# Kernel optimization log

Measured on AMD Instinct MI355X. Metric: run time of the kernel, lower is better.

Reference implementation:

```python
import jax, jax.numpy as jnp
import numpy as np

B, P, L1, D = 64, 16, 16, 1024  # images, people/img, object slots/img (slot0=no-object), feat dim
SP = 32   # flattened spatial (Conv_spatial output channels)
PROJ = 512
ACT = 29


def setup_inputs() -> dict:
    key = jax.random.key(0)
    ks = jax.random.split(key, 16)
    rn = lambda k, s, sc=1.0: jax.random.normal(k, s, dtype=jnp.float32) * sc
    w = 0.02  # weight init scale
    return {
        "people": rn(ks[0], (B, P, D)),
        "objects": rn(ks[1], (B, L1, D)),
        "context": rn(ks[2], (B, D)),
        "spatial": rn(ks[3], (B, P * L1, SP)),
        "Wvis_w": rn(ks[4], (3 * D, PROJ), w), "Wvis_b": jnp.zeros((PROJ,), jnp.float32),
        "Wspat_w": rn(ks[5], (SP, PROJ), w), "Wspat_b": jnp.zeros((PROJ,), jnp.float32),
        "Wip_w": rn(ks[6], (PROJ, 1), w), "Wip_b": jnp.zeros((1,), jnp.float32),
        "Wref_w": rn(ks[7], (PROJ, ACT), w), "Wref_b": jnp.zeros((ACT,), jnp.float32),
        "Watt_w": rn(ks[8], (PROJ, ACT), w), "Watt_b": jnp.zeros((ACT,), jnp.float32),
        "Woh_w": rn(ks[9], (D, D), w), "Woh_b": jnp.zeros((D,), jnp.float32),
        "Who_w": rn(ks[10], (D, D), w), "Who_b": jnp.zeros((D,), jnp.float32),
        "Wg_w": rn(ks[11], (2 * D, ACT), w), "Wg_b": jnp.zeros((ACT,), jnp.float32),
    }


def reference(people, objects, context, spatial,
              Wvis_w, Wvis_b, Wspat_w, Wspat_b, Wip_w, Wip_b,
              Wref_w, Wref_b, Watt_w, Watt_b,
              Woh_w, Woh_b, Who_w, Who_b, Wg_w, Wg_b):
    Bn, Pn, Dn = people.shape
    L = objects.shape[1]
    C = Bn * Pn * L

    # --- ROI.pairing: all (person, object-slot) pairs + image context -> [C, 3D]
    pe = jnp.broadcast_to(people[:, :, None, :], (Bn, Pn, L, Dn))
    ob = jnp.broadcast_to(objects[:, None, :, :], (Bn, Pn, L, Dn))
    cx = jnp.broadcast_to(context[:, None, None, :], (Bn, Pn, L, Dn))
    pairs = jnp.concatenate([pe, ob, cx], axis=-1).reshape(C, 3 * Dn)

    # --- attention / visual projection heads
    a_ho = jax.nn.relu(spatial.reshape(C, -1) @ Wspat_w + Wspat_b)   # W_Spat
    f_vis = jax.nn.relu(pairs @ Wvis_w + Wvis_b)                     # W_vis
    f_ref = f_vis * a_ho
    i_ho = f_ref @ Wip_w + Wip_b                                     # [C,1]
    interaction_prob = jax.nn.sigmoid(i_ho)
    p_ref = f_ref @ Wref_w + Wref_b                                  # [C,29]
    p_att = a_ho @ Watt_w + Watt_b                                   # [C,29]

    # --- graph message passing: adjacency = interaction probs, skipping slot 0 (no-object)
    adj = interaction_prob.reshape(Bn, Pn, L)[:, :, 1:]              # [B,P,O]
    oh = jax.nn.relu(objects[:, 1:] @ Woh_w + Woh_b)                 # W_oh on objects
    ho = jax.nn.relu(people @ Who_w + Who_b)                         # W_ho on people
    people_r = people + jnp.einsum('bpo,bod->bpd', adj, oh)
    objects_r = objects[:, 1:] + jnp.einsum('bpo,bpd->bod', adj, ho)
    objects_full = jnp.concatenate([objects[:, :1], objects_r], axis=1)  # re-attach no-object slot

    # --- refined all-pairs concat -> W_graph
    pe_r = jnp.broadcast_to(people_r[:, :, None, :], (Bn, Pn, L, Dn))
    ob_r = jnp.broadcast_to(objects_full[:, None, :, :], (Bn, Pn, L, Dn))
    pairs_g = jnp.concatenate([pe_r, ob_r], axis=-1).reshape(C, 2 * Dn)
    p_graph = pairs_g @ Wg_w + Wg_b                                  # [C,29]

    return (i_ho, p_ref, p_att, p_graph)
```

## Files before the change

### kernel.cpp

```cpp
#include <hip/hip_runtime.h>


typedef unsigned short u16;
typedef short s16x8 __attribute__((ext_vector_type(8)));
typedef float f32x4 __attribute__((ext_vector_type(4)));

__device__ __forceinline__ u16 f2b(float f) {
    union { float f; unsigned int i; } v; v.f = f;
    unsigned int r = (v.i + 0x7fffu + ((v.i >> 16) & 1u)) >> 16;
    return (u16)r;
}
__device__ __forceinline__ float b2f(u16 u) {
    union { float f; unsigned int i; } v; v.i = ((unsigned int)u) << 16; return v.f;
}
__device__ __forceinline__ unsigned int pack2(float x, float y) {
    return (unsigned int)f2b(x) | ((unsigned int)f2b(y) << 16);
}

#define OFF_WSPATT 0u
#define OFF_WREFT  32768u
#define OFF_WATTT  65536u
#define OFF_WGT    98304u
#define OFF_PP     229376u
#define OFF_PO     1277952u
#define OFF_PC     2326528u
#define OFF_ADJ    2392064u
#define OFF_HP     2457600u
#define OFF_HOF    2588672u
#define OFF_YH     2719744u
#define OFF_ZO     2850816u
#define ZERO_OFF   2457600u
#define ZERO_LEN   516096u
#define OFF_WVIST2 2973696u
#define OFF_WHOT2  6119424u
#define OFF_WOHT2  8216576u
#define OFF_PEOB   10313728u
#define OFF_OBJB   12410880u
#define OFF_CTXB   14508032u
#define OFF_SPATB  14639104u
#define OFF_AHOB   15687680u

__global__ __launch_bounds__(256) void prep_all(
    const float* __restrict__ people, const float* __restrict__ objects,
    const float* __restrict__ context, const float* __restrict__ spatial,
    const float* __restrict__ Wvis, const float* __restrict__ Who,
    const float* __restrict__ Woh, const float* __restrict__ Wspat,
    const float* __restrict__ Wref, const float* __restrict__ Watt,
    const float* __restrict__ Wg,
    u16* __restrict__ peoB, u16* __restrict__ objB, u16* __restrict__ ctxB,
    u16* __restrict__ spatB, u16* __restrict__ WvisT, u16* __restrict__ WhoT,
    u16* __restrict__ WohT, u16* __restrict__ WspatT, u16* __restrict__ WrefT,
    u16* __restrict__ WattT, u16* __restrict__ WgT, float* __restrict__ zeroWS)
{
    __shared__ float S[64][65];
    int bid = blockIdx.x, t = threadIdx.x;
    if (bid < 896) {
        const float* src; u16* dst; int N, K, kt, nt;
        int tb = bid;
        if (tb < 256)      { src = Who;  dst = WhoT;  K = 1024; N = 1024; kt = tb >> 4; nt = tb & 15; }
        else if (tb < 512) { tb -= 256; src = Woh;  dst = WohT;  K = 1024; N = 1024; kt = tb >> 4; nt = tb & 15; }
        else               { tb -= 512; src = Wvis; dst = WvisT; K = 3072; N = 512;  kt = tb >> 3; nt = tb & 7; }
        int k0 = kt * 64, n0 = nt * 64;
        int r = t >> 4, c4 = (t & 15) * 4;
#pragma unroll
        for (int i = 0; i < 4; i++) {
            float4 v = *(const float4*)&src[(size_t)(k0 + r + 16 * i) * N + n0 + c4];
            S[r + 16 * i][c4 + 0] = v.x;
            S[r + 16 * i][c4 + 1] = v.y;
            S[r + 16 * i][c4 + 2] = v.z;
            S[r + 16 * i][c4 + 3] = v.w;
        }
        __syncthreads();
#pragma unroll
        for (int i = 0; i < 4; i++) {
            int nn = r + 16 * i;
            unsigned int lo = pack2(S[c4 + 0][nn], S[c4 + 1][nn]);
            unsigned int hi = pack2(S[c4 + 2][nn], S[c4 + 3][nn]);
            *(uint2*)&dst[(size_t)(n0 + nn) * K + k0 + c4] = make_uint2(lo, hi);
        }
        return;
    }
    int g = (bid - 896) * 256 + t;
    const int gsz = 512 * 256;
    for (int i = g; i < 262144; i += gsz) {
        float4 v = ((const float4*)people)[i];
        ((uint2*)peoB)[i] = make_uint2(pack2(v.x, v.y), pack2(v.z, v.w));
    }
    for (int i = g; i < 262144; i += gsz) {
        float4 v = ((const float4*)objects)[i];
        ((uint2*)objB)[i] = make_uint2(pack2(v.x, v.y), pack2(v.z, v.w));
    }
    for (int i = g; i < 16384; i += gsz) {
        float4 v = ((const float4*)context)[i];
        ((uint2*)ctxB)[i] = make_uint2(pack2(v.x, v.y), pack2(v.z, v.w));
    }
    for (int i = g; i < 131072; i += gsz) {
        float4 v = ((const float4*)spatial)[i];
        ((uint2*)spatB)[i] = make_uint2(pack2(v.x, v.y), pack2(v.z, v.w));
    }
    for (int i = g; i < 32256; i += gsz) {
        f32x4 z = {0.f, 0.f, 0.f, 0.f};
        ((f32x4*)zeroWS)[i] = z;
    }
    for (int i = g; i < 512 * 32; i += gsz) {
        int n = i >> 5, k = i & 31;
        WspatT[i] = f2b(Wspat[k * 512 + n]);
    }
    for (int i = g; i < 32 * 512; i += gsz) {
        int n = i >> 9, k = i & 511;
        WrefT[i] = (n < 29) ? f2b(Wref[k * 29 + n]) : (u16)0;
        WattT[i] = (n < 29) ? f2b(Watt[k * 29 + n]) : (u16)0;
    }
    for (int i = g; i < 32 * 2048; i += gsz) {
        int n = i >> 11, k = i & 2047;
        WgT[i] = (n < 29) ? f2b(Wg[k * 29 + n]) : (u16)0;
    }
}

__global__ __launch_bounds__(256) void fused_gemms(
    const u16* __restrict__ peoB, const u16* __restrict__ objB,
    const u16* __restrict__ ctxB, const u16* __restrict__ WvisT,
    const u16* __restrict__ WhoT, const float* __restrict__ Who_b,
    const u16* __restrict__ WohT, const float* __restrict__ Woh_b,
    const u16* __restrict__ WgT,
    const u16* __restrict__ spatB, const u16* __restrict__ WspatT,
    const float* __restrict__ bspat,
    const u16* __restrict__ WattT, const float* __restrict__ batt,
    u16* __restrict__ Pp, u16* __restrict__ Po, u16* __restrict__ Pc,
    float* __restrict__ Yh, float* __restrict__ Zo,
    float* __restrict__ Hp, float* __restrict__ HoF,
    u16* __restrict__ ahoB, float* __restrict__ outAtt)
{
    __shared__ __align__(16) unsigned char LB[36864];
    u16 (*As)[64][72] = (u16(*)[64][72])LB;
    u16 (*Bs)[64][72] = (u16(*)[64][72])(LB + 18432);

    int b0 = blockIdx.x, bid;
    if (b0 < 264)      bid = (b0 & 7) * 33 + (b0 >> 3);
    else if (b0 < 760) { int l = b0 - 264; bid = 264 + (l & 7) * 62 + (l >> 3); }
    else if (b0 < 888) { int l = b0 - 760; bid = 760 + (l & 7) * 16 + (l >> 3); }
    else               { int l = b0 - 888; bid = 888 + (l & 7) * 64 + (l >> 3); }
    int t = threadIdx.x;
    int lane = t & 63, w = t >> 6;
    int l16 = lane & 15, q = lane >> 4;
    int wy = w >> 1, wx = w & 1;

    if (bid < 760) {
        const u16 *Ap, *Bp;
        int Bstride, bm, bn, koff = 0, zrm = 0;
        u16* outB = nullptr;
        const float* bb = nullptr; const u16* Wg2 = nullptr; float* U = nullptr;
        if (bid < 264) {
            int bx = bid & 7, ty = bid >> 3;
            if (ty < 16)      { Ap = peoB; outB = Pp; koff = 0;    bm = ty * 64; }
            else if (ty < 32) { Ap = objB; outB = Po; koff = 1024; bm = (ty - 16) * 64; }
            else              { Ap = ctxB; outB = Pc; koff = 2048; bm = 0; }
            bn = bx * 64;
            Bp = WvisT; Bstride = 3072;
        } else {
            int r3 = bid - 264;
            int zz, rt, nbt;
            if (r3 < 256) { zz = 0; rt = r3 >> 4; nbt = r3 & 15; }
            else          { zz = 1; r3 -= 256; rt = r3 >> 4; nbt = r3 & 15; }
            zrm = zz;
            Ap = zz ? objB : peoB;
            Bp = zz ? WohT : WhoT; Bstride = 1024;
            bb = zz ? Woh_b : Who_b;
            Wg2 = zz ? WgT : WgT + 1024;
            U = zz ? Zo : Yh;
            bm = rt * 64; bn = nbt * 64;
        }

        int tr = t >> 3, tc = (t & 7) * 8;
        int a0r = bm + tr, a1r = bm + 32 + tr;
        if (zrm) { a0r = (a0r / 15) * 16 + (a0r % 15) + 1;
                   a1r = (a1r / 15) * 16 + (a1r % 15) + 1; }
        const u16* gA0 = Ap + (size_t)a0r * 1024 + tc;
        const u16* gA1 = Ap + (size_t)a1r * 1024 + tc;
        const u16* gB0 = Bp + (size_t)(bn + tr) * Bstride + koff + tc;
        const u16* gB1 = Bp + (size_t)(bn + 32 + tr) * Bstride + koff + tc;

        s16x8 rA0 = *(const s16x8*)gA0, rA1 = *(const s16x8*)gA1;
        s16x8 rB0 = *(const s16x8*)gB0, rB1 = *(const s16x8*)gB1;
        gA0 += 64; gA1 += 64; gB0 += 64; gB1 += 64;
        *(s16x8*)&As[0][tr][tc]      = rA0;
        *(s16x8*)&As[0][32 + tr][tc] = rA1;
        *(s16x8*)&Bs[0][tr][tc]      = rB0;
        *(s16x8*)&Bs[0][32 + tr][tc] = rB1;
        rA0 = *(const s16x8*)gA0; rA1 = *(const s16x8*)gA1;
        rB0 = *(const s16x8*)gB0; rB1 = *(const s16x8*)gB1;
        gA0 += 64; gA1 += 64; gB0 += 64; gB1 += 64;
        __syncthreads();

        f32x4 acc00 = {0,0,0,0}, acc01 = {0,0,0,0}, acc10 = {0,0,0,0}, acc11 = {0,0,0,0};
        int cur = 0;
        for (int kt = 0; kt < 16; kt++) {
#pragma unroll
            for (int kk = 0; kk < 2; kk++) {
                s16x8 a0 = *(const s16x8*)&As[cur][wy * 32 + l16][kk * 32 + q * 8];
                s16x8 a1 = *(const s16x8*)&As[cur][wy * 32 + 16 + l16][kk * 32 + q * 8];
                s16x8 b0 = *(const s16x8*)&Bs[cur][wx * 32 + l16][kk * 32 + q * 8];
                s16x8 b1 = *(const s16x8*)&Bs[cur][wx * 32 + 16 + l16][kk * 32 + q * 8];
                acc00 = __builtin_amdgcn_mfma_f32_16x16x32_bf16(a0, b0, acc00, 0, 0, 0);
                acc01 = __builtin_amdgcn_mfma_f32_16x16x32_bf16(a0, b1, acc01, 0, 0, 0);
                acc10 = __builtin_amdgcn_mfma_f32_16x16x32_bf16(a1, b0, acc10, 0, 0, 0);
                acc11 = __builtin_amdgcn_mfma_f32_16x16x32_bf16(a1, b1, acc11, 0, 0, 0);
            }
            if (kt < 15) {
                __syncthreads();
                *(s16x8*)&As[cur ^ 1][tr][tc]      = rA0;
                *(s16x8*)&As[cur ^ 1][32 + tr][tc] = rA1;
                *(s16x8*)&Bs[cur ^ 1][tr][tc]      = rB0;
                *(s16x8*)&Bs[cur ^ 1][32 + tr][tc] = rB1;
                if (kt < 14) {
                    rA0 = *(const s16x8*)gA0; rA1 = *(const s16x8*)gA1;
                    rB0 = *(const s16x8*)gB0; rB1 = *(const s16x8*)gB1;
                    gA0 += 64; gA1 += 64; gB0 += 64; gB1 += 64;
                }
                __syncthreads();
                cur ^= 1;
            }
        }

        f32x4 accs[2][2] = {{acc00, acc01}, {acc10, acc11}};
        if (bid < 264) {
#pragma unroll
            for (int ii = 0; ii < 2; ii++)
#pragma unroll
                for (int jj = 0; jj < 2; jj++) {
                    int col = bn + wx * 32 + jj * 16 + l16;
#pragma unroll
                    for (int r = 0; r < 4; r++) {
                        int row = bm + wy * 32 + ii * 16 + q * 4 + r;
                        outB[(size_t)row * 512 + col] = f2b(accs[ii][jj][r]);
                    }
                }
        } else {
            u16 (*T)[72] = As[0];
#pragma unroll
            for (int ii = 0; ii < 2; ii++)
#pragma unroll
                for (int jj = 0; jj < 2; jj++) {
                    int col = wx * 32 + jj * 16 + l16;
                    float bv = bb[bn + col];
#pragma unroll
                    for (int rr = 0; rr < 4; rr++) {
                        float v = accs[ii][jj][rr] + bv;
                        T[wy * 32 + ii * 16 + q * 4 + rr][col] = f2b(fmaxf(v, 0.f));
                    }
                }
            __syncthreads();

            f32x4 s20 = {0,0,0,0}, s21 = {0,0,0,0};
#pragma unroll
            for (int kk = 0; kk < 64; kk += 32) {
                s16x8 a2 = *(const s16x8*)(&T[w * 16 + l16][kk + q * 8]);
                s16x8 b20 = *(const s16x8*)(Wg2 + (size_t)l16 * 2048 + bn + kk + q * 8);
                s16x8 b21 = *(const s16x8*)(Wg2 + (size_t)(16 + l16) * 2048 + bn + kk + q * 8);
                s20 = __builtin_amdgcn_mfma_f32_16x16x32_bf16(a2, b20, s20, 0, 0, 0);
                s21 = __builtin_amdgcn_mfma_f32_16x16x32_bf16(a2, b21, s21, 0, 0, 0);
            }
#pragma unroll
            for (int rr = 0; rr < 4; rr++) {
                int row = bm + w * 16 + q * 4 + rr;
                atomicAdd(&U[(size_t)row * 32 + l16], s20[rr]);
                atomicAdd(&U[(size_t)row * 32 + 16 + l16], s21[rr]);
            }
        }
    } else if (bid < 888) {
        int r3 = bid - 760;
        int bx = r3 & 7, by = (r3 >> 3) & 7, z = r3 >> 6;
        const u16* A  = z ? objB : peoB;
        const u16* BT = z ? WgT + 1024 : WgT;
        float* outF   = z ? HoF : Hp;
        int bm = bx * 128 + w * 32;
        int kb = by * 128;
        const u16* ap0 = A + (size_t)(bm + l16) * 1024 + kb + q * 8;
        const u16* ap1 = A + (size_t)(bm + 16 + l16) * 1024 + kb + q * 8;
        const u16* bp0 = BT + (size_t)l16 * 2048 + kb + q * 8;
        const u16* bp1 = BT + (size_t)(16 + l16) * 2048 + kb + q * 8;
        f32x4 acc00 = {0,0,0,0}, acc01 = {0,0,0,0}, acc10 = {0,0,0,0}, acc11 = {0,0,0,0};
        s16x8 bA0[4], bA1[4], bB0[4], bB1[4];
#pragma unroll
        for (int s = 0; s < 4; s++) {
            bA0[s] = *(const s16x8*)(ap0 + s * 32);
            bA1[s] = *(const s16x8*)(ap1 + s * 32);
            bB0[s] = *(const s16x8*)(bp0 + s * 32);
            bB1[s] = *(const s16x8*)(bp1 + s * 32);
        }
#pragma unroll
        for (int s = 0; s < 4; s++) {
            acc00 = __builtin_amdgcn_mfma_f32_16x16x32_bf16(bA0[s], bB0[s], acc00, 0, 0, 0);
            acc01 = __builtin_amdgcn_mfma_f32_16x16x32_bf16(bA0[s], bB1[s], acc01, 0, 0, 0);
            acc10 = __builtin_amdgcn_mfma_f32_16x16x32_bf16(bA1[s], bB0[s], acc10, 0, 0, 0);
            acc11 = __builtin_amdgcn_mfma_f32_16x16x32_bf16(bA1[s], bB1[s], acc11, 0, 0, 0);
        }
        f32x4 accs[2][2] = {{acc00, acc01}, {acc10, acc11}};
#pragma unroll
        for (int ii = 0; ii < 2; ii++)
#pragma unroll
            for (int jj = 0; jj < 2; jj++)
#pragma unroll
                for (int r = 0; r < 4; r++)
                    atomicAdd(&outF[(size_t)(bm + ii * 16 + q * 4 + r) * 32 + jj * 16 + l16],
                              accs[ii][jj][r]);
    } else {
        u16 (*tile)[512] = (u16(*)[512])LB;
        int c0 = (bid - 888) * 32;

        {
            s16x8 a0 = *(const s16x8*)(spatB + (size_t)(c0 + l16) * 32 + q * 8);
            s16x8 a1 = *(const s16x8*)(spatB + (size_t)(c0 + 16 + l16) * 32 + q * 8);
            const u16* wb = WspatT + (size_t)(w * 128 + l16) * 32 + q * 8;
            s16x8 cb = *(const s16x8*)wb;
            s16x8 nb_ = *(const s16x8*)(wb + 16 * 32);
            wb += 32 * 32;
#pragma unroll
            for (int nt = 0; nt < 8; nt++) {
                s16x8 tb;
                if (nt < 6) { tb = *(const s16x8*)wb; wb += 16 * 32; }
                int n = w * 128 + nt * 16;
                f32x4 acc0 = {0,0,0,0}, acc1 = {0,0,0,0};
                acc0 = __builtin_amdgcn_mfma_f32_16x16x32_bf16(a0, cb, acc0, 0, 0, 0);
                acc1 = __builtin_amdgcn_mfma_f32_16x16x32_bf16(a1, cb, acc1, 0, 0, 0);
                cb = nb_; nb_ = tb;
                float bias = bspat[n + l16];
#pragma unroll
                for (int r = 0; r < 4; r++) {
                    tile[q * 4 + r][n + l16]      = f2b(fmaxf(acc0[r] + bias, 0.f));
                    tile[16 + q * 4 + r][n + l16] = f2b(fmaxf(acc1[r] + bias, 0.f));
                }
            }
        }
        __syncthreads();

        {
            int rt = w >> 1, ct = w & 1;
            const u16* bp = WattT + (size_t)(ct * 16 + l16) * 512 + q * 8;
            const u16* ar = &tile[rt * 16 + l16][q * 8];
            f32x4 acc0 = {0,0,0,0}, acc1 = {0,0,0,0}, acc2 = {0,0,0,0}, acc3 = {0,0,0,0};
#pragma unroll
            for (int s = 0; s < 16; s += 4) {
                s16x8 a0 = *(const s16x8*)(ar + (s + 0) * 32);
                s16x8 a1 = *(const s16x8*)(ar + (s + 1) * 32);
                s16x8 a2 = *(const s16x8*)(ar + (s + 2) * 32);
                s16x8 a3 = *(const s16x8*)(ar + (s + 3) * 32);
                s16x8 b0 = *(const s16x8*)(bp + (s + 0) * 32);
                s16x8 b1 = *(const s16x8*)(bp + (s + 1) * 32);
                s16x8 b2 = *(const s16x8*)(bp + (s + 2) * 32);
                s16x8 b3 = *(const s16x8*)(bp + (s + 3) * 32);
                acc0 = __builtin_amdgcn_mfma_f32_16x16x32_bf16(a0, b0, acc0, 0, 0, 0);
                acc1 = __builtin_amdgcn_mfma_f32_16x16x32_bf16(a1, b1, acc1, 0, 0, 0);
                acc2 = __builtin_amdgcn_mfma_f32_16x16x32_bf16(a2, b2, acc2, 0, 0, 0);
                acc3 = __builtin_amdgcn_mfma_f32_16x16x32_bf16(a3, b3, acc3, 0, 0, 0);
            }
            f32x4 acc = (acc0 + acc1) + (acc2 + acc3);
            int col = ct * 16 + l16;
            if (col < 29) {
                float bias = batt[col];
#pragma unroll
                for (int r = 0; r < 4; r++) {
                    int row = c0 + rt * 16 + q * 4 + r;
                    outAtt[(size_t)row * 29 + col] = acc[r] + bias;
                }
            }
        }

        {
            const uint4* ts = (const uint4*)tile;
            uint4* gd = (uint4*)(ahoB + (size_t)c0 * 512);
            for (int i = t; i < 2048; i += 256) gd[i] = ts[i];
        }
    }
}

__global__ __launch_bounds__(256) void mega(
    const u16* __restrict__ ahoB,
    const u16* __restrict__ Pp, const u16* __restrict__ Po,
    const u16* __restrict__ Pc, const float* __restrict__ bvis,
    const u16* __restrict__ WrefT, const float* __restrict__ bref,
    const float* __restrict__ wip, const float* __restrict__ bip,
    float* __restrict__ outI, float* __restrict__ outRef,
    float* __restrict__ adjw)
{
    __shared__ u16 tile[32][512];
    __shared__ float part[32][8];
    __shared__ float wipS[512];
    int t = threadIdx.x;
    int b0 = blockIdx.x;
    int bid = (b0 & 7) * 64 + (b0 >> 3);
    int c0 = bid * 32;
    int lane = t & 63, w = t >> 6;
    int l16 = lane & 15, q = lane >> 4;

    {
        float2 u = *(const float2*)(wip + t * 2);
        wipS[t * 2]     = u.x;
        wipS[t * 2 + 1] = u.y;
    }
    __syncthreads();

    {
        int row = t >> 3, g = t & 7;
        int c = c0 + row;
        int rp = c >> 4, bimg = c >> 8;
        int ro = bimg * 16 + (c & 15);
        const u16* ppr = Pp + (size_t)rp * 512;
        const u16* por = Po + (size_t)ro * 512;
        const u16* pcr = Pc + (size_t)bimg * 512;
        const u16* ahr = ahoB + (size_t)c * 512;
        float ps = 0.f;
#pragma unroll 4
        for (int j = 0; j < 64; j += 2) {
            int col = g * 64 + j;
            unsigned int upp = *(const unsigned int*)(ppr + col);
            unsigned int upo = *(const unsigned int*)(por + col);
            unsigned int upc = *(const unsigned int*)(pcr + col);
            float2 bv = *(const float2*)(bvis + col);
            unsigned int uah = *(const unsigned int*)(ahr + col);
            float fv0 = fmaxf(b2f((u16)(upp & 0xffff)) + b2f((u16)(upo & 0xffff))
                            + b2f((u16)(upc & 0xffff)) + bv.x, 0.f);
            float fv1 = fmaxf(b2f((u16)(upp >> 16)) + b2f((u16)(upo >> 16))
                            + b2f((u16)(upc >> 16)) + bv.y, 0.f);
            float fr0 = fv0 * b2f((u16)(uah & 0xffff));
            float fr1 = fv1 * b2f((u16)(uah >> 16));
            *(unsigned int*)(&tile[row][col]) = pack2(fr0, fr1);
            ps += fr0 * wipS[col] + fr1 * wipS[col + 1];
        }
        part[row][g] = ps;
    }
    __syncthreads();

    if (t < 32) {
        float s = part[t][0] + part[t][1] + part[t][2] + part[t][3]
                + part[t][4] + part[t][5] + part[t][6] + part[t][7] + bip[0];
        outI[c0 + t] = s;
        adjw[c0 + t] = 1.f / (1.f + expf(-s));
    }

    {
        int rt = w >> 1, ct = w & 1;
        const u16* bp = WrefT + (size_t)(ct * 16 + l16) * 512 + q * 8;
        const u16* ar = &tile[rt * 16 + l16][q * 8];
        f32x4 acc0 = {0,0,0,0}, acc1 = {0,0,0,0}, acc2 = {0,0,0,0}, acc3 = {0,0,0,0};
#pragma unroll
        for (int s = 0; s < 16; s += 4) {
            s16x8 a0 = *(const s16x8*)(ar + (s + 0) * 32);
            s16x8 a1 = *(const s16x8*)(ar + (s + 1) * 32);
            s16x8 a2 = *(const s16x8*)(ar + (s + 2) * 32);
            s16x8 a3 = *(const s16x8*)(ar + (s + 3) * 32);
            s16x8 b0 = *(const s16x8*)(bp + (s + 0) * 32);
            s16x8 b1 = *(const s16x8*)(bp + (s + 1) * 32);
            s16x8 b2 = *(const s16x8*)(bp + (s + 2) * 32);
            s16x8 b3 = *(const s16x8*)(bp + (s + 3) * 32);
            acc0 = __builtin_amdgcn_mfma_f32_16x16x32_bf16(a0, b0, acc0, 0, 0, 0);
            acc1 = __builtin_amdgcn_mfma_f32_16x16x32_bf16(a1, b1, acc1, 0, 0, 0);
            acc2 = __builtin_amdgcn_mfma_f32_16x16x32_bf16(a2, b2, acc2, 0, 0, 0);
            acc3 = __builtin_amdgcn_mfma_f32_16x16x32_bf16(a3, b3, acc3, 0, 0, 0);
        }
        f32x4 acc = (acc0 + acc1) + (acc2 + acc3);
        int col = ct * 16 + l16;
        if (col < 29) {
            float bias = bref[col];
#pragma unroll
            for (int r = 0; r < 4; r++) {
                int row = c0 + rt * 16 + q * 4 + r;
                outRef[(size_t)row * 29 + col] = acc[r] + bias;
            }
        }
    }
}

__global__ __launch_bounds__(256) void pgraph2(
    const float* __restrict__ adjw, const float* __restrict__ Hp,
    const float* __restrict__ HoF, const float* __restrict__ Yh,
    const float* __restrict__ Zo, const float* __restrict__ bg,
    float* __restrict__ outG)
{
    int b = blockIdx.x, t = threadIdx.x;
    __shared__ float adjS[16][16];
    __shared__ float YhS[16][32];
    __shared__ float ZoS[15][32];
    __shared__ float PA[16][32];
    __shared__ float OA[16][32];
    adjS[t >> 4][t & 15] = adjw[b * 256 + t];
    for (int i = t; i < 512; i += 256)
        YhS[i >> 5][i & 31] = Yh[(size_t)(b * 16 + (i >> 5)) * 32 + (i & 31)];
    for (int i = t; i < 480; i += 256)
        ZoS[i >> 5][i & 31] = Zo[(size_t)(b * 15 + (i >> 5)) * 32 + (i & 31)];
    __syncthreads();
    for (int i = t; i < 512; i += 256) {
        int p = i >> 5, j = i & 31;
        float s = 0.f;
#pragma unroll
        for (int o = 0; o < 15; o++) s += adjS[p][o + 1] * ZoS[o][j];
        PA[p][j] = s;
        float s2 = 0.f;
#pragma unroll
        for (int pp = 0; pp < 16; pp++) s2 += adjS[pp][p] * YhS[pp][j];
        OA[p][j] = s2;
    }
    __syncthreads();
    int p = t >> 4, l = t & 15;
    const float* hp = Hp + (size_t)(b * 16 + p) * 32;
    const float* ho = HoF + (size_t)(b * 16 + l) * 32;
    size_t c = (size_t)b * 256 + t;
    for (int j = 0; j < 29; j++) {
        float v = hp[j] + ho[j] + bg[j] + PA[p][j];
        if (l >= 1) v += OA[l][j];
        outG[c * 29 + j] = v;
    }
}

extern "C" void kernel_launch(void* const* d_in, const int* in_sizes, int n_in,
                              void* d_out, int out_size, void* d_ws, size_t ws_size,
                              hipStream_t stream)
{
    const float* people  = (const float*)d_in[0];
    const float* objects = (const float*)d_in[1];
    const float* context = (const float*)d_in[2];
    const float* spatial = (const float*)d_in[3];
    const float* Wvis_w  = (const float*)d_in[4];
    const float* Wvis_b  = (const float*)d_in[5];
    const float* Wspat_w = (const float*)d_in[6];
    const float* Wspat_b = (const float*)d_in[7];
    const float* Wip_w   = (const float*)d_in[8];
    const float* Wip_b   = (const float*)d_in[9];
    const float* Wref_w  = (const float*)d_in[10];
    const float* Wref_b  = (const float*)d_in[11];
    const float* Watt_w  = (const float*)d_in[12];
    const float* Watt_b  = (const float*)d_in[13];
    const float* Woh_w   = (const float*)d_in[14];
    const float* Woh_b   = (const float*)d_in[15];
    const float* Who_w   = (const float*)d_in[16];
    const float* Who_b   = (const float*)d_in[17];
    const float* Wg_w    = (const float*)d_in[18];
    const float* Wg_b    = (const float*)d_in[19];

    char* ws = (char*)d_ws;
    u16* WspatT = (u16*)(ws + OFF_WSPATT);
    u16* WrefT  = (u16*)(ws + OFF_WREFT);
    u16* WattT  = (u16*)(ws + OFF_WATTT);
    u16* WgT    = (u16*)(ws + OFF_WGT);
    u16* Ppb    = (u16*)(ws + OFF_PP);
    u16* Pob    = (u16*)(ws + OFF_PO);
    u16* Pcb    = (u16*)(ws + OFF_PC);
    float* adjw = (float*)(ws + OFF_ADJ);
    float* Hp   = (float*)(ws + OFF_HP);
    float* HoF  = (float*)(ws + OFF_HOF);
    float* Yh   = (float*)(ws + OFF_YH);
    float* Zo   = (float*)(ws + OFF_ZO);
    u16* WvisT2 = (u16*)(ws + OFF_WVIST2);
    u16* WhoT2  = (u16*)(ws + OFF_WHOT2);
    u16* WohT2  = (u16*)(ws + OFF_WOHT2);
    u16* peoB   = (u16*)(ws + OFF_PEOB);
    u16* objB   = (u16*)(ws + OFF_OBJB);
    u16* ctxB   = (u16*)(ws + OFF_CTXB);
    u16* spatB  = (u16*)(ws + OFF_SPATB);
    u16* ahoB   = (u16*)(ws + OFF_AHOB);
    float* zeroWS = (float*)(ws + ZERO_OFF);

    float* outI   = (float*)d_out;
    float* outRef = outI + 16384;
    float* outAtt = outI + 491520;
    float* outG   = outI + 966656;

    prep_all<<<1408, 256, 0, stream>>>(people, objects, context, spatial,
        Wvis_w, Who_w, Woh_w, Wspat_w, Wref_w, Watt_w, Wg_w,
        peoB, objB, ctxB, spatB, WvisT2, WhoT2, WohT2,
        WspatT, WrefT, WattT, WgT, zeroWS);

    fused_gemms<<<1400, 256, 0, stream>>>(peoB, objB, ctxB, WvisT2,
        WhoT2, Who_b, WohT2, Woh_b, WgT,
        spatB, WspatT, Wspat_b, WattT, Watt_b,
        Ppb, Pob, Pcb, Yh, Zo, Hp, HoF,
        ahoB, outAtt);

    mega<<<512, 256, 0, stream>>>(ahoB,
                                  Ppb, Pob, Pcb, Wvis_b,
                                  WrefT, Wref_b,
                                  Wip_w, Wip_b,
                                  outI, outRef, adjw);

    pgraph2<<<64, 256, 0, stream>>>(adjw, Hp, HoF, Yh, Zo, Wg_b, outG);
}
```

Before: 156.6 us.

## Stage GEMM tiles via direct global-to-LDS loads with XOR-swizzled layout

Replaces the register-staged double-buffered GEMM loads in the main fused_gemms path with global_load_lds direct copies into LDS. The padded 72-column layout becomes an unpadded 64-column layout with an XOR swizzle, which is meant to avoid bank conflicts and save LDS. This cuts register pressure and VGPR round-trips and removes one barrier per k-step. It relies on the async load having completed by the single __syncthreads, which is a correctness risk if no explicit vmcnt wait is emitted.

```diff
diff --git a/kernel.cpp b/kernel.cpp
--- a/kernel.cpp
+++ b/kernel.cpp
@@ -15,6 +15,12 @@
 }
 __device__ __forceinline__ unsigned int pack2(float x, float y) {
     return (unsigned int)f2b(x) | ((unsigned int)f2b(y) << 16);
+}
+
+typedef __attribute__((address_space(1))) const unsigned int GU1;
+typedef __attribute__((address_space(3))) unsigned int LU3;
+__device__ __forceinline__ void gld_lds16(const u16* g, u16* l) {
+    __builtin_amdgcn_global_load_lds((GU1*)g, (LU3*)l, 16, 0, 0);
 }
 
 #define OFF_WSPATT 0u
@@ -131,9 +137,7 @@
     float* __restrict__ Hp, float* __restrict__ HoF,
     u16* __restrict__ ahoB, float* __restrict__ outAtt)
 {
-    __shared__ __align__(16) unsigned char LB[36864];
-    u16 (*As)[64][72] = (u16(*)[64][72])LB;
-    u16 (*Bs)[64][72] = (u16(*)[64][72])(LB + 18432);
+    __shared__ __align__(16) unsigned char LB[32768];
 
     int b0 = blockIdx.x, bid;
     if (b0 < 264)      bid = (b0 & 7) * 33 + (b0 >> 3);
@@ -171,56 +175,65 @@
             bm = rt * 64; bn = nbt * 64;
         }
 
-        int tr = t >> 3, tc = (t & 7) * 8;
-        int a0r = bm + tr, a1r = bm + 32 + tr;
-        if (zrm) { a0r = (a0r / 15) * 16 + (a0r % 15) + 1;
-                   a1r = (a1r / 15) * 16 + (a1r % 15) + 1; }
-        const u16* gA0 = Ap + (size_t)a0r * 1024 + tc;
-        const u16* gA1 = Ap + (size_t)a1r * 1024 + tc;
-        const u16* gB0 = Bp + (size_t)(bn + tr) * Bstride + koff + tc;
-        const u16* gB1 = Bp + (size_t)(bn + 32 + tr) * Bstride + koff + tc;
-
-        s16x8 rA0 = *(const s16x8*)gA0, rA1 = *(const s16x8*)gA1;
-        s16x8 rB0 = *(const s16x8*)gB0, rB1 = *(const s16x8*)gB1;
-        gA0 += 64; gA1 += 64; gB0 += 64; gB1 += 64;
-        *(s16x8*)&As[0][tr][tc]      = rA0;
-        *(s16x8*)&As[0][32 + tr][tc] = rA1;
-        *(s16x8*)&Bs[0][tr][tc]      = rB0;
-        *(s16x8*)&Bs[0][32 + tr][tc] = rB1;
-        rA0 = *(const s16x8*)gA0; rA1 = *(const s16x8*)gA1;
-        rB0 = *(const s16x8*)gB0; rB1 = *(const s16x8*)gB1;
-        gA0 += 64; gA1 += 64; gB0 += 64; gB1 += 64;
+        u16* A0 = (u16*)LB;
+        u16* A1 = (u16*)(LB + 8192);
+        u16* B0 = (u16*)(LB + 16384);
+        u16* B1 = (u16*)(LB + 24576);
+
+        int lj = lane >> 3;
+        int swl = ((lane & 7) ^ lj) * 8;
+        int rA[2], rB[2];
+#pragma unroll
+        for (int jj = 0; jj < 2; jj++) {
+            int rloc = 16 * w + 8 * jj + lj;
+            int ga = bm + rloc;
+            if (zrm) ga = (ga / 15) * 16 + (ga % 15) + 1;
+            rA[jj] = ga;
+            rB[jj] = bn + rloc;
+        }
+
+#define STAGE_TILE(AB, BB, KT)                                                 \
+        {                                                                      \
+            int ko = (KT) * 64;                                                \
+            _Pragma("unroll")                                                  \
+            for (int jj = 0; jj < 2; jj++) {                                   \
+                gld_lds16(Ap + (size_t)rA[jj] * 1024 + ko + swl,               \
+                          (AB) + (16 * w + 8 * jj) * 64);                      \
+                gld_lds16(Bp + (size_t)rB[jj] * Bstride + koff + ko + swl,     \
+                          (BB) + (16 * w + 8 * jj) * 64);                      \
+            }                                                                  \
+        }
+
+        STAGE_TILE(A0, B0, 0)
         __syncthreads();
 
+        int sw16 = (l16 & 7) << 4;
         f32x4 acc00 = {0,0,0,0}, acc01 = {0,0,0,0}, acc10 = {0,0,0,0}, acc11 = {0,0,0,0};
-        int cur = 0;
         for (int kt = 0; kt < 16; kt++) {
+            u16* Ac = (kt & 1) ? A1 : A0;
+            u16* Bc = (kt & 1) ? B1 : B0;
+            if (kt < 15) {
+                u16* An = (kt & 1) ? A0 : A1;
+                u16* Bn = (kt & 1) ? B0 : B1;
+                STAGE_TILE(An, Bn, kt + 1)
+            }
+            const char* Ab = (const char*)Ac;
+            const char* Bb = (const char*)Bc;
 #pragma unroll
             for (int kk = 0; kk < 2; kk++) {
-                s16x8 a0 = *(const s16x8*)&As[cur][wy * 32 + l16][kk * 32 + q * 8];
-                s16x8 a1 = *(const s16x8*)&As[cur][wy * 32 + 16 + l16][kk * 32 + q * 8];
-                s16x8 b0 = *(const s16x8*)&Bs[cur][wx * 32 + l16][kk * 32 + q * 8];
-                s16x8 b1 = *(const s16x8*)&Bs[cur][wx * 32 + 16 + l16][kk * 32 + q * 8];
+                int cbs = (kk * 64 + q * 16) ^ sw16;
+                s16x8 a0 = *(const s16x8*)(Ab + (wy * 32 + l16) * 128 + cbs);
+                s16x8 a1 = *(const s16x8*)(Ab + (wy * 32 + 16 + l16) * 128 + cbs);
+                s16x8 b0 = *(const s16x8*)(Bb + (wx * 32 + l16) * 128 + cbs);
+                s16x8 b1 = *(const s16x8*)(Bb + (wx * 32 + 16 + l16) * 128 + cbs);
                 acc00 = __builtin_amdgcn_mfma_f32_16x16x32_bf16(a0, b0, acc00, 0, 0, 0);
                 acc01 = __builtin_amdgcn_mfma_f32_16x16x32_bf16(a0, b1, acc01, 0, 0, 0);
                 acc10 = __builtin_amdgcn_mfma_f32_16x16x32_bf16(a1, b0, acc10, 0, 0, 0);
                 acc11 = __builtin_amdgcn_mfma_f32_16x16x32_bf16(a1, b1, acc11, 0, 0, 0);
             }
-            if (kt < 15) {
-                __syncthreads();
-                *(s16x8*)&As[cur ^ 1][tr][tc]      = rA0;
-                *(s16x8*)&As[cur ^ 1][32 + tr][tc] = rA1;
-                *(s16x8*)&Bs[cur ^ 1][tr][tc]      = rB0;
-                *(s16x8*)&Bs[cur ^ 1][32 + tr][tc] = rB1;
-                if (kt < 14) {
-                    rA0 = *(const s16x8*)gA0; rA1 = *(const s16x8*)gA1;
-                    rB0 = *(const s16x8*)gB0; rB1 = *(const s16x8*)gB1;
-                    gA0 += 64; gA1 += 64; gB0 += 64; gB1 += 64;
-                }
-                __syncthreads();
-                cur ^= 1;
-            }
-        }
+            __syncthreads();
+        }
+#undef STAGE_TILE
 
         f32x4 accs[2][2] = {{acc00, acc01}, {acc10, acc11}};
         if (bid < 264) {
@@ -236,25 +249,30 @@
                     }
                 }
         } else {
-            u16 (*T)[72] = As[0];
+            char* T = (char*)A0;
 #pragma unroll
             for (int ii = 0; ii < 2; ii++)
 #pragma unroll
                 for (int jj = 0; jj < 2; jj++) {
-                    int col = wx * 32 + jj * 16 + l16;
-                    float bv = bb[bn + col];
+                    int colb = (wx * 32 + jj * 16 + l16) * 2;
+                    float bv = bb[bn + wx * 32 + jj * 16 + l16];
 #pragma unroll
                     for (int rr = 0; rr < 4; rr++) {
+                        int rowT = wy * 32 + ii * 16 + q * 4 + rr;
                         float v = accs[ii][jj][rr] + bv;
-                        T[wy * 32 + ii * 16 + q * 4 + rr][col] = f2b(fmaxf(v, 0.f));
+                        *(u16*)(T + rowT * 128 + (colb ^ ((rowT & 7) << 4)))
+                            = f2b(fmaxf(v, 0.f));
                     }
                 }
             __syncthreads();
 
             f32x4 s20 = {0,0,0,0}, s21 = {0,0,0,0};
+            int row2 = w * 16 + l16;
+            int sw2 = (l16 & 7) << 4;
 #pragma unroll
             for (int kk = 0; kk < 64; kk += 32) {
-                s16x8 a2 = *(const s16x8*)(&T[w * 16 + l16][kk + q * 8]);
+                s16x8 a2 = *(const s16x8*)((const char*)T + row2 * 128
+                                           + ((kk * 2 + q * 16) ^ sw2));
                 s16x8 b20 = *(const s16x8*)(Wg2 + (size_t)l16 * 2048 + bn + kk + q * 8);
                 s16x8 b21 = *(const s16x8*)(Wg2 + (size_t)(16 + l16) * 2048 + bn + kk + q * 8);
                 s20 = __builtin_amdgcn_mfma_f32_16x16x32_bf16(a2, b20, s20, 0, 0, 0);
```

New measurement: 158.1 us. Within noise of the previous version (+1.0%).
